# Optimization experiments

Hardware: AMD Instinct MI355X
Metric: run time of the kernel (lower is better)

Reference implementation:

```python
import jax, jax.numpy as jnp
import numpy as np

B, N, H, D = 4, 2048, 16, 64
FEATS = H * D  # 1024; module scales scores by sqrt(feats), not sqrt(head_dim)


def setup_inputs() -> dict:
    key = jax.random.key(0)
    ks = jax.random.split(key, 9)
    s = 1.0 / np.sqrt(D)
    return {
        "x": jax.random.normal(ks[0], (B, N, H, D), dtype=jnp.float32),
        "Wq": jax.random.uniform(ks[1], (H, D, D), jnp.float32, -s, s),
        "bq": jax.random.uniform(ks[2], (H, D), jnp.float32, -s, s),
        "Wk": jax.random.uniform(ks[3], (H, D, D), jnp.float32, -s, s),
        "bk": jax.random.uniform(ks[4], (H, D), jnp.float32, -s, s),
        "Wv": jax.random.uniform(ks[5], (H, D, D), jnp.float32, -s, s),
        "bv": jax.random.uniform(ks[6], (H, D), jnp.float32, -s, s),
        "Wo": jax.random.uniform(ks[7], (H, D, D), jnp.float32, -s, s),
        "bo": jax.random.uniform(ks[8], (H, D), jnp.float32, -s, s),
    }


def reference(x, Wq, bq, Wk, bk, Wv, bv, Wo, bo):
    # per-head linears as one batched einsum: [b,n,h,d] x [h,d,o] -> [b,n,h,o]
    q = jnp.einsum("bnhd,hdo->bnho", x, Wq) + bq
    k = jnp.einsum("bnhd,hdo->bnho", x, Wk) + bk
    v = jnp.einsum("bnhd,hdo->bnho", x, Wv) + bv
    sqrt_d = jnp.asarray(FEATS, x.dtype) ** 0.5  # sqrt(feats) per original code
    # scores: [b,h,i,j]
    score = jax.nn.softmax(jnp.einsum("bihf,bjhf->bhij", q, k) / sqrt_d, axis=-1)
    attn = jnp.einsum("bhij,bjhf->bihf", score, v)  # [b,n,h,d]
    out = jnp.einsum("bnhd,hdo->bnho", attn, Wo) + bo
    return out
```

## Files before the change

### kernel.cpp

```cpp
#include <hip/hip_runtime.h>

#define Bsz  4
#define Nseq 2048
#define Hn   16
#define Dh   64
#define BH   (Bsz*Hn)
#define NT32 (Nseq/32)

#define AS1 __attribute__((address_space(1)))
#define AS3 __attribute__((address_space(3)))

typedef __attribute__((ext_vector_type(8))) short bf16x8;
typedef __attribute__((ext_vector_type(16))) float f32x16;
typedef __attribute__((ext_vector_type(4))) float f32x4;
typedef __attribute__((ext_vector_type(2))) float f32x2;
typedef __attribute__((ext_vector_type(4))) unsigned short u16x4;

#define MFMA32 __builtin_amdgcn_mfma_f32_32x32x16_bf16

static __device__ __forceinline__ unsigned short f2bf(float f) {
    unsigned u = __float_as_uint(f);
    u = (u + 0x7fffu + ((u >> 16) & 1u)) >> 16;
    return (unsigned short)u;
}
static __device__ __forceinline__ float bf2f(unsigned short s) {
    return __uint_as_float((unsigned)s << 16);
}
static __device__ __forceinline__ unsigned cvt_pk_bf16(float lo, float hi) {
    unsigned r;
    asm("v_cvt_pk_bf16_f32 %0, %1, %2" : "=v"(r) : "v"(lo), "v"(hi));
    return r;
}
static __device__ __forceinline__ void swap32(unsigned &a, unsigned &b) {
    asm("v_permlane32_swap_b32 %0, %1" : "+v"(a), "+v"(b));
}
static __device__ __forceinline__ float exp2v(float x) {
    float r;
    asm("v_exp_f32 %0, %1" : "=v"(r) : "v"(x));
    return r;
}
static __device__ __forceinline__ f32x2 pk_add(f32x2 a, f32x2 b) {
    f32x2 d;
    asm("v_pk_add_f32 %0, %1, %2" : "=v"(d) : "v"(a), "v"(b));
    return d;
}

__global__ __launch_bounds__(256) void wprep_kernel(
    const float* __restrict__ Wq, const float* __restrict__ Wk,
    const float* __restrict__ Wv,
    unsigned short* __restrict__ gWtH, unsigned short* __restrict__ gWtL)
{
    __shared__ float ws[64][65];
    const int mh = blockIdx.x;
    const int m = mh >> 4, h = mh & 15;
    const int tid = threadIdx.x;
    const float* W = (m == 0 ? Wq : (m == 1 ? Wk : Wv)) + h * 4096;

    for (int c = tid; c < 1024; c += 256) {
        int row = c >> 4, col = (c & 15) * 4;
        *(f32x4*)&ws[row][col] = *(const f32x4*)&W[row * 64 + col];
    }
    __syncthreads();

    const int o = tid >> 2, dblk = (tid & 3) * 16;
    size_t base = ((size_t)mh * 64 + o) * 64 + dblk;
#pragma unroll
    for (int i4 = 0; i4 < 4; ++i4) {
        u16x4 vh, vl;
#pragma unroll
        for (int j = 0; j < 4; ++j) {
            float v = ws[dblk + i4 * 4 + j][o];
            unsigned short hh = f2bf(v);
            vh[j] = hh;
            vl[j] = f2bf(v - bf2f(hh));
        }
        *(u16x4*)&gWtH[base + i4 * 4] = vh;
        *(u16x4*)&gWtL[base + i4 * 4] = vl;
    }
}

__global__ __launch_bounds__(256) void proj_kernel(
    const float* __restrict__ x,
    const unsigned short* __restrict__ gWtH, const unsigned short* __restrict__ gWtL,
    const float* __restrict__ bq, const float* __restrict__ bk,
    const float* __restrict__ bv,
    unsigned short* __restrict__ gQ, unsigned short* __restrict__ gK,
    unsigned short* __restrict__ gVt)
{
    const int bh = blockIdx.x, h = bh & (Hn - 1), b = bh >> 4;
    const int n0 = blockIdx.y * 64;
    const int tid = threadIdx.x;
    const int w = tid >> 6, lane = tid & 63, l31 = lane & 31, l5 = lane >> 5;
    const int qi = w >> 1, oj = w & 1;

    const int nrow = n0 + qi * 32 + l31;
    const float* xrow = x + (((size_t)b * Nseq + nrow) * Hn + h) * Dh;

    bf16x8 xh[4], xl[4];
#pragma unroll
    for (int ks = 0; ks < 4; ++ks) {
        f32x4 v0 = *(const f32x4*)&xrow[ks * 16 + l5 * 8];
        f32x4 v1 = *(const f32x4*)&xrow[ks * 16 + l5 * 8 + 4];
#pragma unroll
        for (int e = 0; e < 4; ++e) {
            unsigned short h0 = f2bf(v0[e]);
            xh[ks][e] = (short)h0;
            xl[ks][e] = (short)f2bf(v0[e] - bf2f(h0));
            unsigned short h1 = f2bf(v1[e]);
            xh[ks][4 + e] = (short)h1;
            xl[ks][4 + e] = (short)f2bf(v1[e] - bf2f(h1));
        }
    }

    const int o = oj * 32 + l31;

    f32x16 acc[3] = {};
#pragma unroll
    for (int m = 0; m < 3; ++m) {
        const unsigned short* WH = gWtH + (((size_t)m * 16 + h) * 64 + o) * 64;
        const unsigned short* WL = gWtL + (((size_t)m * 16 + h) * 64 + o) * 64;
#pragma unroll
        for (int ks = 0; ks < 4; ++ks) {
            bf16x8 wh = *(const bf16x8*)&WH[ks * 16 + l5 * 8];
            bf16x8 wl = *(const bf16x8*)&WL[ks * 16 + l5 * 8];
            if (m < 2) {
                acc[m] = MFMA32(xh[ks], wh, acc[m], 0, 0, 0);
                acc[m] = MFMA32(xl[ks], wh, acc[m], 0, 0, 0);
                acc[m] = MFMA32(xh[ks], wl, acc[m], 0, 0, 0);
            } else {
                acc[2] = MFMA32(wh, xh[ks], acc[2], 0, 0, 0);
                acc[2] = MFMA32(wl, xh[ks], acc[2], 0, 0, 0);
                acc[2] = MFMA32(wh, xl[ks], acc[2], 0, 0, 0);
            }
        }
    }

    {
        float bias = bq[h * 64 + o];
#pragma unroll
        for (int r = 0; r < 16; ++r) {
            int nl = (r & 3) + 8 * (r >> 2) + 4 * l5;
            int n = n0 + qi * 32 + nl;
            gQ[((size_t)bh * Nseq + n) * Dh + o] =
                f2bf((acc[0][r] + bias) * 0.0450842200f);
        }
    }
    {
        float bias = bk[h * 64 + o];
#pragma unroll
        for (int r = 0; r < 16; ++r) {
            int nl = (r & 3) + 8 * (r >> 2) + 4 * l5;
            int n = n0 + qi * 32 + nl;
            int c = (((o >> 3) ^ (n & 7)) * 8) + (o & 7);
            gK[((size_t)bh * Nseq + n) * Dh + c] = f2bf(acc[1][r] + bias);
        }
    }
    {
        const int tile = (n0 >> 5) + qi;
        const int kt = l31;
#pragma unroll
        for (int r = 0; r < 16; ++r) {
            int ol = (r & 3) + 8 * (r >> 2) + 4 * l5;
            int ov = oj * 32 + ol;
            float bias = bv[h * 64 + ov];
            int c = (((kt >> 3) ^ ((ov >> 2) & 3)) * 8) + (kt & 7);
            gVt[(((size_t)bh * NT32 + tile) * 64 + ov) * 32 + c] =
                f2bf(acc[2][r] + bias);
        }
    }
}

__global__ __launch_bounds__(256, 4) void flash_kernel(
    const unsigned short* __restrict__ gQ,
    const unsigned short* __restrict__ gK,
    const unsigned short* __restrict__ gVt,
    const float* __restrict__ Wo, const float* __restrict__ bo,
    float* __restrict__ out)
{
    __shared__ unsigned short kbuf[4][2048];
    __shared__ unsigned short vbuf[2][2048];

    const int bh = blockIdx.x, h = bh & (Hn - 1), b = bh >> 4;
    const int tid = threadIdx.x;
    const int w = tid >> 6, lane = tid & 63;
    const int l31 = lane & 31, l5 = lane >> 5;
    const int qrow = blockIdx.y * 128 + w * 32 + l31;

    bf16x8 qf[4];
#pragma unroll
    for (int kk = 0; kk < 4; ++kk)
        qf[kk] = *(const bf16x8*)&gQ[((size_t)bh * Nseq + qrow) * Dh + kk * 16 + l5 * 8];

    float z0 = 0.f;
    asm volatile("" : "+v"(z0));
    f32x16 zc = {z0, z0, z0, z0, z0, z0, z0, z0, z0, z0, z0, z0, z0, z0, z0, z0};

    f32x16 acc[2] = {};
    float l = 0.f;

    auto stageK = [&](int t, int slot) {
        const unsigned short* src = gK + ((size_t)bh * Nseq + (size_t)t * 32) * Dh + tid * 8;
        __builtin_amdgcn_global_load_lds((const AS1 void*)src,
                                         (AS3 void*)(&kbuf[slot][w * 512]), 16, 0, 0);
    };
    auto stageV = [&](int t, int slot) {
        const unsigned short* src = gVt + ((size_t)(bh * NT32 + t)) * 2048 + tid * 8;
        __builtin_amdgcn_global_load_lds((const AS1 void*)src,
                                         (AS3 void*)(&vbuf[slot][w * 512]), 16, 0, 0);
    };

    auto qk_tile = [&](const unsigned short* __restrict__ kb) -> f32x16 {
        const int roff = l31 * 64;
        const int sw = l31 & 7;
        bf16x8 kf = *(const bf16x8*)&kb[roff + ((l5 ^ sw) * 8)];
        f32x16 s = MFMA32(kf, qf[0], zc, 0, 0, 0);
#pragma unroll
        for (int kk = 1; kk < 4; ++kk) {
            kf = *(const bf16x8*)&kb[roff + (((kk * 2 + l5) ^ sw) * 8)];
            s = MFMA32(kf, qf[kk], s, 0, 0, 0);
        }
        return s;
    };

    auto soft_pv = [&](f32x16& s, const unsigned short* __restrict__ vb) {
#pragma unroll
        for (int r = 0; r < 16; ++r) s[r] = exp2v(s[r]);
        f32x2* sp = (f32x2*)&s;
        f32x2 u0 = pk_add(sp[0], sp[1]), u1 = pk_add(sp[2], sp[3]);
        f32x2 u2 = pk_add(sp[4], sp[5]), u3 = pk_add(sp[6], sp[7]);
        u0 = pk_add(u0, u1); u2 = pk_add(u2, u3);
        u0 = pk_add(u0, u2);
        l += u0[0] + u0[1];
#pragma unroll
        for (int ks = 0; ks < 2; ++ks) {
            const int b0 = 8 * ks;
            unsigned x0 = cvt_pk_bf16(s[b0 + 0], s[b0 + 1]);
            unsigned x1 = cvt_pk_bf16(s[b0 + 2], s[b0 + 3]);
            unsigned y0 = cvt_pk_bf16(s[b0 + 4], s[b0 + 5]);
            unsigned y1 = cvt_pk_bf16(s[b0 + 6], s[b0 + 7]);
            swap32(x0, y0);
            swap32(x1, y1);
            bf16x8 pf;
            ((unsigned*)&pf)[0] = x0; ((unsigned*)&pf)[1] = x1;
            ((unsigned*)&pf)[2] = y0; ((unsigned*)&pf)[3] = y1;
#pragma unroll
            for (int dt = 0; dt < 2; ++dt) {
                const int row = dt * 32 + l31;
                bf16x8 vf = *(const bf16x8*)&vb[row * 32 + (((ks * 2 + l5) ^ ((row >> 2) & 3)) * 8)];
                acc[dt] = MFMA32(vf, pf, acc[dt], 0, 0, 0);
            }
        }
    };

    stageK(0, 0);
    stageV(0, 0);
    stageK(1, 1);
    __syncthreads();
    f32x16 sA = qk_tile(kbuf[0]);
    f32x16 sB;

#pragma unroll 1
    for (int tb = 0; tb < NT32; tb += 4) {
        __syncthreads();
        stageK(min(tb + 2, NT32 - 1), 2);
        stageV(min(tb + 1, NT32 - 1), 1);
        sB = qk_tile(kbuf[1]);
        soft_pv(sA, vbuf[0]);
        __syncthreads();
        stageK(min(tb + 3, NT32 - 1), 3);
        stageV(min(tb + 2, NT32 - 1), 0);
        sA = qk_tile(kbuf[2]);
        soft_pv(sB, vbuf[1]);
        __syncthreads();
        stageK(min(tb + 4, NT32 - 1), 0);
        stageV(min(tb + 3, NT32 - 1), 1);
        sB = qk_tile(kbuf[3]);
        soft_pv(sA, vbuf[0]);
        __syncthreads();
        stageK(min(tb + 5, NT32 - 1), 1);
        stageV(min(tb + 4, NT32 - 1), 0);
        sA = qk_tile(kbuf[0]);
        soft_pv(sB, vbuf[1]);
    }

    __syncthreads();
    {
        unsigned short* wl = &kbuf[0][0];
        for (int c = tid; c < 512; c += 256) {
            int o = c >> 3, c8 = c & 7;
            int cc = ((c8 ^ (o & 7)) * 8);
#pragma unroll
            for (int jj = 0; jj < 4; ++jj) wl[o * 64 + cc + jj]     = f2bf(Wo[(h * 64 + c8 * 8 + jj) * 64 + o]);
#pragma unroll
            for (int jj = 0; jj < 4; ++jj) wl[o * 64 + cc + 4 + jj] = f2bf(Wo[(h * 64 + c8 * 8 + 4 + jj) * 64 + o]);
        }
    }
    __syncthreads();

    l += __shfl_xor(l, 32);
    float inv = 1.f / l;
#pragma unroll
    for (int dt = 0; dt < 2; ++dt)
#pragma unroll
        for (int r = 0; r < 16; ++r) acc[dt][r] *= inv;

    const unsigned short* wot = &kbuf[0][0];
    f32x16 oc[2] = {};
#pragma unroll
    for (int kk = 0; kk < 4; ++kk) {
        const int dt = kk >> 1;
        const int b0 = 8 * (kk & 1);
        unsigned x0 = cvt_pk_bf16(acc[dt][b0 + 0], acc[dt][b0 + 1]);
        unsigned x1 = cvt_pk_bf16(acc[dt][b0 + 2], acc[dt][b0 + 3]);
        unsigned y0 = cvt_pk_bf16(acc[dt][b0 + 4], acc[dt][b0 + 5]);
        unsigned y1 = cvt_pk_bf16(acc[dt][b0 + 6], acc[dt][b0 + 7]);
        swap32(x0, y0);
        swap32(x1, y1);
        bf16x8 af;
        ((unsigned*)&af)[0] = x0; ((unsigned*)&af)[1] = x1;
        ((unsigned*)&af)[2] = y0; ((unsigned*)&af)[3] = y1;
#pragma unroll
        for (int ot = 0; ot < 2; ++ot) {
            int row = ot * 32 + l31;
            bf16x8 wf = *(const bf16x8*)&wot[row * 64 + (((kk * 2 + l5) ^ (row & 7)) * 8)];
            oc[ot] = MFMA32(wf, af, oc[ot], 0, 0, 0);
        }
    }

    float* obase = out + (((size_t)b * Nseq + qrow) * Hn + h) * Dh;
#pragma unroll
    for (int ot = 0; ot < 2; ++ot)
#pragma unroll
        for (int rq = 0; rq < 4; ++rq) {
            int o = ot * 32 + rq * 8 + l5 * 4;
            f32x4 bb = *(const f32x4*)&bo[h * 64 + o];
            f32x4 vv;
            vv[0] = oc[ot][rq * 4 + 0] + bb[0];
            vv[1] = oc[ot][rq * 4 + 1] + bb[1];
            vv[2] = oc[ot][rq * 4 + 2] + bb[2];
            vv[3] = oc[ot][rq * 4 + 3] + bb[3];
            *(f32x4*)&obase[o] = vv;
        }
}

extern "C" void kernel_launch(void* const* d_in, const int* in_sizes, int n_in,
                              void* d_out, int out_size, void* d_ws, size_t ws_size,
                              hipStream_t stream) {
    const float* x  = (const float*)d_in[0];
    const float* Wq = (const float*)d_in[1];
    const float* bq = (const float*)d_in[2];
    const float* Wk = (const float*)d_in[3];
    const float* bk = (const float*)d_in[4];
    const float* Wv = (const float*)d_in[5];
    const float* bv = (const float*)d_in[6];
    const float* Wo = (const float*)d_in[7];
    const float* bo = (const float*)d_in[8];
    float* out = (float*)d_out;

    unsigned short* gQ   = (unsigned short*)d_ws;
    unsigned short* gK   = gQ + (size_t)BH * Nseq * Dh;
    unsigned short* gVt  = gK + (size_t)BH * Nseq * Dh;
    unsigned short* gWtH = gVt + (size_t)BH * Nseq * Dh;
    unsigned short* gWtL = gWtH + (size_t)3 * 16 * 64 * 64;

    wprep_kernel<<<48, 256, 0, stream>>>(Wq, Wk, Wv, gWtH, gWtL);
    proj_kernel<<<dim3(BH, Nseq / 64), 256, 0, stream>>>(x, gWtH, gWtL, bq, bk, bv, gQ, gK, gVt);
    flash_kernel<<<dim3(BH, Nseq / 128), 256, 0, stream>>>(gQ, gK, gVt, Wo, bo, out);
}
```

Before: 131.1 us.

## Stage K and V in 64-row windows with double buffering in flash kernel

Restructures the flash attention main loop from a 32-row K/V pipeline with a skewed 4-slot K ring and 2-slot V ring to 64-row windows that are double-buffered. Each window loads K and V together, computes two QK tiles, then two softmax-PV steps. This halves the number of barriers per key and simplifies the staging. In exchange it drops the overlap of one QK tile's MFMAs with the previous softmax, and LDS use rises from 24KB to 32KB per block, which may limit occupancy at 4 blocks per CU.

```diff
diff --git a/kernel.cpp b/kernel.cpp
--- a/kernel.cpp
+++ b/kernel.cpp
@@ -5,6 +5,7 @@
 #define Hn   16
 #define Dh   64
 #define BH   (Bsz*Hn)
+#define NT64 (Nseq/64)
 #define NT32 (Nseq/32)
 
 #define AS1 __attribute__((address_space(1)))
@@ -177,8 +178,8 @@
     const float* __restrict__ Wo, const float* __restrict__ bo,
     float* __restrict__ out)
 {
-    __shared__ unsigned short kbuf[4][2048];
-    __shared__ unsigned short vbuf[2][2048];
+    __shared__ unsigned short kbuf[2][4096];
+    __shared__ unsigned short vbuf[2][4096];
 
     const int bh = blockIdx.x, h = bh & (Hn - 1), b = bh >> 4;
     const int tid = threadIdx.x;
@@ -198,15 +199,17 @@
     f32x16 acc[2] = {};
     float l = 0.f;
 
-    auto stageK = [&](int t, int slot) {
-        const unsigned short* src = gK + ((size_t)bh * Nseq + (size_t)t * 32) * Dh + tid * 8;
-        __builtin_amdgcn_global_load_lds((const AS1 void*)src,
-                                         (AS3 void*)(&kbuf[slot][w * 512]), 16, 0, 0);
-    };
-    auto stageV = [&](int t, int slot) {
-        const unsigned short* src = gVt + ((size_t)(bh * NT32 + t)) * 2048 + tid * 8;
-        __builtin_amdgcn_global_load_lds((const AS1 void*)src,
-                                         (AS3 void*)(&vbuf[slot][w * 512]), 16, 0, 0);
+    auto stage = [&](int t, int bufi) {
+        const unsigned short* ks = gK + ((size_t)bh * Nseq + (size_t)t * 64) * Dh;
+        const unsigned short* vs = gVt + ((size_t)(bh * NT32 + 2 * t)) * 2048;
+#pragma unroll
+        for (int i = 0; i < 2; ++i) {
+            int off = w * 1024 + i * 512 + lane * 8;
+            __builtin_amdgcn_global_load_lds((const AS1 void*)(ks + off),
+                                             (AS3 void*)(&kbuf[bufi][w * 1024 + i * 512]), 16, 0, 0);
+            __builtin_amdgcn_global_load_lds((const AS1 void*)(vs + off),
+                                             (AS3 void*)(&vbuf[bufi][w * 1024 + i * 512]), 16, 0, 0);
+        }
     };
 
     auto qk_tile = [&](const unsigned short* __restrict__ kb) -> f32x16 {
@@ -252,35 +255,24 @@
         }
     };
 
-    stageK(0, 0);
-    stageV(0, 0);
-    stageK(1, 1);
-    __syncthreads();
-    f32x16 sA = qk_tile(kbuf[0]);
-    f32x16 sB;
+    auto window_step = [&](const unsigned short* __restrict__ kb,
+                           const unsigned short* __restrict__ vb) {
+        f32x16 sA = qk_tile(kb);
+        f32x16 sB = qk_tile(kb + 2048);
+        soft_pv(sA, vb);
+        soft_pv(sB, vb + 2048);
+    };
+
+    stage(0, 0);
 
 #pragma unroll 1
-    for (int tb = 0; tb < NT32; tb += 4) {
+    for (int t2 = 0; t2 < NT64; t2 += 2) {
         __syncthreads();
-        stageK(min(tb + 2, NT32 - 1), 2);
-        stageV(min(tb + 1, NT32 - 1), 1);
-        sB = qk_tile(kbuf[1]);
-        soft_pv(sA, vbuf[0]);
+        stage(t2 + 1, 1);
+        window_step(&kbuf[0][0], &vbuf[0][0]);
         __syncthreads();
-        stageK(min(tb + 3, NT32 - 1), 3);
-        stageV(min(tb + 2, NT32 - 1), 0);
-        sA = qk_tile(kbuf[2]);
-        soft_pv(sB, vbuf[1]);
-        __syncthreads();
-        stageK(min(tb + 4, NT32 - 1), 0);
-        stageV(min(tb + 3, NT32 - 1), 1);
-        sB = qk_tile(kbuf[3]);
-        soft_pv(sA, vbuf[0]);
-        __syncthreads();
-        stageK(min(tb + 5, NT32 - 1), 1);
-        stageV(min(tb + 4, NT32 - 1), 0);
-        sA = qk_tile(kbuf[0]);
-        soft_pv(sB, vbuf[1]);
+        if (t2 + 2 < NT64) stage(t2 + 2, 0);
+        window_step(&kbuf[1][0], &vbuf[1][0]);
     }
 
     __syncthreads();
```

Result: faster. 126.2 us (-3.8%).
